# Optimization experiments

Measured on AMD Instinct MI355X. Metric: run time of the kernel, lower is better.

## Reference

```python
import jax, jax.numpy as jnp
import numpy as np

B, T, H, W = 4, 8, 256, 256


def _shift(u, axis, d):
    """Value at index i comes from i+d along `axis`; zero (Dirichlet) boundary."""
    if d == 0:
        return u
    pad = [(0, 0)] * u.ndim
    sl = [slice(None)] * u.ndim
    if d > 0:
        sl[axis] = slice(d, None)
        pad[axis] = (0, d)
    else:
        sl[axis] = slice(None, d)
        pad[axis] = (-d, 0)
    return jnp.pad(u[tuple(sl)], pad)


def custom_sigmoid(x, mn, mx):
    # matches NLL.custom_sigmoid: (sigmoid(x) + min/(max-min)) * (max-min)
    return (jax.nn.sigmoid(x) + mn / (mx - mn)) * (mx - mn)


def setup_inputs() -> dict:
    key = jax.random.key(0)
    k1, k2 = jax.random.split(key)
    x = jax.random.normal(k1, (B, T, H, W), dtype=jnp.float32)
    conv_w = jax.random.normal(k2, (8 * T, T, 3, 3), dtype=jnp.float32) * 0.05
    return {"x": x, "conv_w": conv_w}


def reference(x, conv_w):
    Bn, Tn, Hn, Wn = x.shape
    dt = dx = dy = 1.0  # st_lag = [1,1,1]

    # Encoder: Conv2d(n_t -> 8*n_t, 3x3, padding=1, bias=False)
    theta = jax.lax.conv_general_dilated(
        x, conv_w, window_strides=(1, 1), padding="SAME",
        dimension_numbers=("NCHW", "OIHW", "NCHW"))

    # reshape_params: split 8*n_t channels into SPDE fields, bounded to valid ranges
    kappa = custom_sigmoid(theta[:, :Tn], 0.01, 1.0)          # damping
    m1 = theta[:, Tn:2 * Tn]                                   # advection x
    m2 = theta[:, 2 * Tn:3 * Tn]                               # advection y
    Hxx = custom_sigmoid(theta[:, 3 * Tn:4 * Tn], 0.01, 1.0)  # diffusion tensor
    Hxy = 0.1 * jnp.tanh(theta[:, 4 * Tn:5 * Tn])
    Hyx = 0.1 * jnp.tanh(theta[:, 5 * Tn:6 * Tn])
    Hyy = custom_sigmoid(theta[:, 6 * Tn:7 * Tn], 0.01, 1.0)
    tau = custom_sigmoid(theta[:, 7 * Tn:8 * Tn], 0.1, 10.0)   # noise scale

    # finite-difference stencils (zero Dirichlet boundary), vectorized over (B,T)
    def Dx(u):
        return (_shift(u, -1, 1) - _shift(u, -1, -1)) / (2 * dx)

    def Dy(u):
        return (_shift(u, -2, 1) - _shift(u, -2, -1)) / (2 * dy)

    def Dxx(u):
        return (_shift(u, -1, 1) + _shift(u, -1, -1) - 2 * u) / (dx * dx)

    def Dyy(u):
        return (_shift(u, -2, 1) + _shift(u, -2, -1) - 2 * u) / (dy * dy)

    def A(u):
        # advection-diffusion operator: kappa^2 u + m.grad u - div(H grad u)
        return ((kappa * kappa) * u + m1 * Dx(u) + m2 * Dy(u)
                - (Hxx * Dxx(u) + Hyy * Dyy(u) + (Hxy + Hyx) * Dx(Dy(u))))

    # pow=1 -> alpha=2 -> B = A^2 ; M_k = I + dt * B_k
    Mx = x + dt * A(A(x))                      # [B,T,H,W], M_k x_k for all k

    # Q = L^T D L with L block-bidiagonal (L[k,k]=M_k, L[k,k-1]=-I),
    # D_k = diag(dt / tau_k^2)  (inv_tau = sqrt(dt)/tau in create_Q)
    x_prev = jnp.concatenate([jnp.zeros_like(x[:, :1]), x[:, :-1]], axis=1)
    r = Mx - x_prev                            # r_k = M_k x_k - x_{k-1}
    D = dt / (tau * tau)

    xQx = jnp.sum(D * r * r)                   # quadratic form x^T Q x
    logdetD = jnp.sum(jnp.log(D))              # diagonal log-det contribution
    return 0.5 * (xQx - logdetD)
```

## Files before the change

kernel.cpp:

```cpp
#include <hip/hip_runtime.h>

#define F_ELEMS 2097152
#define IMG 65536

typedef _Float16 half8  __attribute__((ext_vector_type(8)));
typedef _Float16 half2v __attribute__((ext_vector_type(2)));
typedef _Float16 half4v __attribute__((ext_vector_type(4)));
typedef float    floatx4 __attribute__((ext_vector_type(4)));

__device__ __forceinline__ float sigm(float x){ return 1.0f/(1.0f + __expf(-x)); }
__device__ __forceinline__ float tanh_fast(float x){
    float t = __expf(2.0f*x);
    return 1.0f - 2.0f/(t + 1.0f);
}

__global__ void zero_out(float* out){ out[0] = 0.0f; }

__global__ __launch_bounds__(256) void conv_mfma(
    const float* __restrict__ x, const float* __restrict__ w,
    _Float16* __restrict__ fld, float* __restrict__ out)
{
    __shared__ _Float16 xt[4*258*8];
    __shared__ _Float16 Wl[12*64*8];
    __shared__ float red[256];

    const int tid = threadIdx.x;
    const int i0  = blockIdx.x << 1;
    const int b   = blockIdx.y;

    for (int e = tid; e < 258*4*4; e += 256){
        int cc = e % 258;
        int rr = (e/258) & 3;
        int cp = e / (258*4);
        int gi = i0 - 1 + rr, gj = cc - 1;
        float v0 = 0.0f, v1 = 0.0f;
        if (gi >= 0 && gi < 256 && gj >= 0 && gj < 256){
            int base = ((b*8 + 2*cp) << 16) + (gi << 8) + gj;
            v0 = x[base];
            v1 = x[base + IMG];
        }
        half2v h; h[0] = (_Float16)v0; h[1] = (_Float16)v1;
        *(half2v*)&xt[(rr*258 + cc)*8 + 2*cp] = h;
    }
    for (int e = tid; e < 12*64*8; e += 256){
        int c  = e & 7;
        int oc = (e >> 3) & 63;
        int t  = e >> 9;
        float v = (t < 9) ? w[(oc*8 + c)*9 + t] : 0.0f;
        Wl[e] = (_Float16)v;
    }
    __syncthreads();

    const int lane = tid & 63;
    const int quad = lane >> 4;
    const int l16  = lane & 15;
    const int wv   = tid >> 6;

    half8 afr[4][3];
    int boff[3];
    #pragma unroll
    for (int s = 0; s < 3; ++s){
        int t  = s*4 + quad;
        afr[0][s] = *(const half8*)&Wl[(t*64 +  0 + l16)*8];
        afr[1][s] = *(const half8*)&Wl[(t*64 + 16 + l16)*8];
        afr[2][s] = *(const half8*)&Wl[(t*64 + 32 + l16)*8];
        afr[3][s] = *(const half8*)&Wl[(t*64 + 48 + l16)*8];
        int tc = (t < 9) ? t : 8;
        int dh = tc / 3, dw = tc - dh*3;
        boff[s] = (dh*258 + dw)*8;
    }

    float ldacc = 0.0f;

    #pragma unroll 2
    for (int it = 0; it < 8; ++it){
        const int g   = it*4 + wv;
        const int r   = g >> 4;
        const int jb  = ((g & 15) << 4) + l16;
        const int xoff = (r*258 + jb)*8;

        floatx4 acc0 = {0,0,0,0}, acc1 = {0,0,0,0}, acc2 = {0,0,0,0}, acc3 = {0,0,0,0};
        #pragma unroll
        for (int s = 0; s < 3; ++s){
            half8 bf = *(const half8*)&xt[xoff + boff[s]];
            acc0 = __builtin_amdgcn_mfma_f32_16x16x32_f16(afr[0][s], bf, acc0, 0, 0, 0);
            acc1 = __builtin_amdgcn_mfma_f32_16x16x32_f16(afr[1][s], bf, acc1, 0, 0, 0);
            acc2 = __builtin_amdgcn_mfma_f32_16x16x32_f16(afr[2][s], bf, acc2, 0, 0, 0);
            acc3 = __builtin_amdgcn_mfma_f32_16x16x32_f16(afr[3][s], bf, acc3, 0, 0, 0);
        }

        const int pix0 = (b << 19) + ((i0 + r) << 8) + jb;
#define STO(f, tt, v) fld[(f)*F_ELEMS + ((tt) << 16) + pix0] = (_Float16)(v)
        #pragma unroll
        for (int rg = 0; rg < 4; ++rg){
            int oc = quad*4 + rg, tt = oc & 7;
            float v = acc0[rg];
            if (oc < 8){ float s = 0.99f*sigm(v) + 0.01f; STO(0, tt, s*s); }
            else       { STO(1, tt, v); }
        }
        #pragma unroll
        for (int rg = 0; rg < 4; ++rg){
            int oc = 16 + quad*4 + rg, tt = oc & 7;
            float v = acc1[rg];
            if (oc < 24){ STO(2, tt, v); }
            else        { STO(3, tt, 0.99f*sigm(v) + 0.01f); }
        }
        #pragma unroll
        for (int rg = 0; rg < 4; ++rg){
            float th    = 0.1f*tanh_fast(acc2[rg]);
            float other = __shfl_xor(th, 32, 64);
            if (quad < 2){
                int tt = quad*4 + rg;
                STO(4, tt, th + other);
            }
        }
        #pragma unroll
        for (int rg = 0; rg < 4; ++rg){
            int oc = 48 + quad*4 + rg, tt = oc & 7;
            float v = acc3[rg];
            if (oc < 56){ STO(5, tt, 0.99f*sigm(v) + 0.01f); }
            else {
                float tau = 9.9f*sigm(v) + 0.1f;
                STO(6, tt, 1.0f/(tau*tau));
                ldacc += __logf(tau);
            }
        }
#undef STO
    }

    red[tid] = ldacc;
    __syncthreads();
    for (int s = 128; s > 0; s >>= 1){
        if (tid < s) red[tid] += red[tid + s];
        __syncthreads();
    }
    if (tid == 0) atomicAdd(out, red[0]);
}

__device__ __forceinline__ void ldf4(const _Float16* __restrict__ p, float o[4]){
    half4v h = *(const half4v*)p;
    o[0] = (float)h[0]; o[1] = (float)h[1]; o[2] = (float)h[2]; o[3] = (float)h[3];
}

__device__ __forceinline__ void row6(const float* __restrict__ u, int rb, int j0, float v[6]){
    const float4 c4 = *(const float4*)&u[rb + j0];
    v[1] = c4.x; v[2] = c4.y; v[3] = c4.z; v[4] = c4.w;
    v[0] = (j0 > 0)   ? u[rb + j0 - 1] : 0.0f;
    v[5] = (j0 < 252) ? u[rb + j0 + 4] : 0.0f;
}

__device__ __forceinline__ void stencil4(const float k2[4], const float m1[4],
    const float m2[4], const float hx[4], const float hs[4], const float hy[4],
    const float vc[6], const float vn[6], const float vs[6], float rp[4])
{
    #pragma unroll
    for (int p = 0; p < 4; ++p){
        float hxx = hx[p], hyy = hy[p];
        rp[p] = (k2[p] + 2.0f*(hxx + hyy))*vc[p+1]
              + (0.5f*m1[p] - hxx)*vc[p+2]
              - (0.5f*m1[p] + hxx)*vc[p]
              + (0.5f*m2[p] - hyy)*vn[p+1]
              - (0.5f*m2[p] + hyy)*vs[p+1]
              - 0.25f*hs[p]*(vn[p+2] - vs[p+2] - vn[p] + vs[p]);
    }
}

#define YSW 268
__global__ __launch_bounds__(256) void fused_A(
    const float* __restrict__ x, const _Float16* __restrict__ fld,
    float* __restrict__ out)
{
    __shared__ float ys[18*YSW];
    __shared__ float red[256];

    const int tid = threadIdx.x;
    const int cg  = tid & 63;
    const int rw  = tid >> 6;
    const int jc  = cg << 2;
    const int bt  = blockIdx.y;
    const int t   = bt & 7;
    const int i0  = blockIdx.x << 4;

    if (tid < 18){ ys[tid*YSW + 3] = 0.0f; ys[tid*YSW + 260] = 0.0f; }

    for (int p = 0; p < 5; ++p){
        int yr = p*4 + rw;
        if (yr < 18){
            int iy = i0 - 1 + yr;
            float y[4] = {0,0,0,0};
            if (iy >= 0 && iy < 256){
                int pix = (bt << 16) + (iy << 8) + jc;
                int rb  = pix - jc;
                float vc[6], vn[6], vs[6];
                row6(x, rb, jc, vc);
                if (iy < 255) row6(x, rb + 256, jc, vn);
                else { vn[0]=vn[1]=vn[2]=vn[3]=vn[4]=vn[5]=0.0f; }
                if (iy > 0) row6(x, rb - 256, jc, vs);
                else { vs[0]=vs[1]=vs[2]=vs[3]=vs[4]=vs[5]=0.0f; }
                float k2[4], m1[4], m2[4], hx[4], hs[4], hy[4];
                ldf4(&fld[0*F_ELEMS + pix], k2);
                ldf4(&fld[1*F_ELEMS + pix], m1);
                ldf4(&fld[2*F_ELEMS + pix], m2);
                ldf4(&fld[3*F_ELEMS + pix], hx);
                ldf4(&fld[4*F_ELEMS + pix], hs);
                ldf4(&fld[5*F_ELEMS + pix], hy);
                stencil4(k2, m1, m2, hx, hs, hy, vc, vn, vs, y);
            }
            float4 y4 = make_float4(y[0], y[1], y[2], y[3]);
            *(float4*)&ys[yr*YSW + 4 + jc] = y4;
        }
    }
    __syncthreads();

    float local = 0.0f;
    #pragma unroll
    for (int p = 0; p < 4; ++p){
        int zr = p*4 + rw;
        int iz = i0 + zr;
        int pix = (bt << 16) + (iz << 8) + jc;
        int base = (zr + 1)*YSW + 4 + jc;

        float vc[6], vn[6], vs[6];
        {
            float4 c4 = *(const float4*)&ys[base];
            vc[1]=c4.x; vc[2]=c4.y; vc[3]=c4.z; vc[4]=c4.w;
            vc[0]=ys[base-1]; vc[5]=ys[base+4];
            float4 n4 = *(const float4*)&ys[base+YSW];
            vn[1]=n4.x; vn[2]=n4.y; vn[3]=n4.z; vn[4]=n4.w;
            vn[0]=ys[base+YSW-1]; vn[5]=ys[base+YSW+4];
            float4 s4 = *(const float4*)&ys[base-YSW];
            vs[1]=s4.x; vs[2]=s4.y; vs[3]=s4.z; vs[4]=s4.w;
            vs[0]=ys[base-YSW-1]; vs[5]=ys[base-YSW+4];
        }
        float k2[4], m1[4], m2[4], hx[4], hs[4], hy[4], dv[4], z[4];
        ldf4(&fld[0*F_ELEMS + pix], k2);
        ldf4(&fld[1*F_ELEMS + pix], m1);
        ldf4(&fld[2*F_ELEMS + pix], m2);
        ldf4(&fld[3*F_ELEMS + pix], hx);
        ldf4(&fld[4*F_ELEMS + pix], hs);
        ldf4(&fld[5*F_ELEMS + pix], hy);
        ldf4(&fld[6*F_ELEMS + pix], dv);
        stencil4(k2, m1, m2, hx, hs, hy, vc, vn, vs, z);

        float4 xc = *(const float4*)&x[pix];
        float4 xp = make_float4(0,0,0,0);
        if (t > 0) xp = *(const float4*)&x[pix - IMG];
        const float* xcp = (const float*)&xc;
        const float* xpp = (const float*)&xp;
        #pragma unroll
        for (int q = 0; q < 4; ++q){
            float r = xcp[q] + z[q] - xpp[q];
            local += dv[q]*r*r;
        }
    }

    red[tid] = local;
    __syncthreads();
    for (int s = 128; s > 0; s >>= 1){
        if (tid < s) red[tid] += red[tid + s];
        __syncthreads();
    }
    if (tid == 0) atomicAdd(out, 0.5f*red[0]);
}

extern "C" void kernel_launch(void* const* d_in, const int* in_sizes, int n_in,
                              void* d_out, int out_size, void* d_ws, size_t ws_size,
                              hipStream_t stream)
{
    const float* x = (const float*)d_in[0];
    const float* w = (const float*)d_in[1];
    float* out = (float*)d_out;
    _Float16* fld = (_Float16*)d_ws;

    zero_out<<<1, 1, 0, stream>>>(out);
    conv_mfma<<<dim3(128, 4), 256, 0, stream>>>(x, w, fld, out);
    fused_A<<<dim3(16, 32), 256, 0, stream>>>(x, fld, out);
}
```

Before: 107.8 us.

## Move log-det into fused kernel, drop zero kernel, use wave-shuffle reductions

Removes the separate zero_out launch by having the first conv block zero the output, and stores tau directly instead of 1/tau^2 so the conv kernel no longer computes logs or runs its shared-memory tree reduction and atomic. The fused stencil kernel now computes 1/tau^2 and accumulates a per-thread product of tau whose log is added to the loss, and replaces its shared-memory tree reduction with wave-level shuffles plus a four-entry shared sum. This trades one launch and two barrier-heavy reductions for extra divides in the second kernel. Zeroing the output inside a block of the conv kernel relies on that kernel finishing before the fused kernel's atomics, which stream ordering guarantees. Storing tau in fp16 and multiplying many taus before the log carries some precision and overflow risk.

```diff
diff --git a/kernel.cpp b/kernel.cpp
--- a/kernel.cpp
+++ b/kernel.cpp
@@ -14,19 +14,18 @@
     return 1.0f - 2.0f/(t + 1.0f);
 }
 
-__global__ void zero_out(float* out){ out[0] = 0.0f; }
-
 __global__ __launch_bounds__(256) void conv_mfma(
     const float* __restrict__ x, const float* __restrict__ w,
     _Float16* __restrict__ fld, float* __restrict__ out)
 {
     __shared__ _Float16 xt[4*258*8];
     __shared__ _Float16 Wl[12*64*8];
-    __shared__ float red[256];
 
     const int tid = threadIdx.x;
     const int i0  = blockIdx.x << 1;
     const int b   = blockIdx.y;
+
+    if (tid == 0 && blockIdx.x == 0 && blockIdx.y == 0) out[0] = 0.0f;
 
     for (int e = tid; e < 258*4*4; e += 256){
         int cc = e % 258;
@@ -70,8 +69,6 @@
         boff[s] = (dh*258 + dw)*8;
     }
 
-    float ldacc = 0.0f;
-
     #pragma unroll 2
     for (int it = 0; it < 8; ++it){
         const int g   = it*4 + wv;
@@ -121,20 +118,11 @@
             if (oc < 56){ STO(5, tt, 0.99f*sigm(v) + 0.01f); }
             else {
                 float tau = 9.9f*sigm(v) + 0.1f;
-                STO(6, tt, 1.0f/(tau*tau));
-                ldacc += __logf(tau);
+                STO(6, tt, tau);
             }
         }
 #undef STO
     }
-
-    red[tid] = ldacc;
-    __syncthreads();
-    for (int s = 128; s > 0; s >>= 1){
-        if (tid < s) red[tid] += red[tid + s];
-        __syncthreads();
-    }
-    if (tid == 0) atomicAdd(out, red[0]);
 }
 
 __device__ __forceinline__ void ldf4(const _Float16* __restrict__ p, float o[4]){
@@ -171,7 +159,7 @@
     float* __restrict__ out)
 {
     __shared__ float ys[18*YSW];
-    __shared__ float red[256];
+    __shared__ float redA[4], redB[4];
 
     const int tid = threadIdx.x;
     const int cg  = tid & 63;
@@ -213,6 +201,7 @@
     __syncthreads();
 
     float local = 0.0f;
+    float lprod = 1.0f;
     #pragma unroll
     for (int p = 0; p < 4; ++p){
         int zr = p*4 + rw;
@@ -232,14 +221,14 @@
             vs[1]=s4.x; vs[2]=s4.y; vs[3]=s4.z; vs[4]=s4.w;
             vs[0]=ys[base-YSW-1]; vs[5]=ys[base-YSW+4];
         }
-        float k2[4], m1[4], m2[4], hx[4], hs[4], hy[4], dv[4], z[4];
+        float k2[4], m1[4], m2[4], hx[4], hs[4], hy[4], tv[4], z[4];
         ldf4(&fld[0*F_ELEMS + pix], k2);
         ldf4(&fld[1*F_ELEMS + pix], m1);
         ldf4(&fld[2*F_ELEMS + pix], m2);
         ldf4(&fld[3*F_ELEMS + pix], hx);
         ldf4(&fld[4*F_ELEMS + pix], hs);
         ldf4(&fld[5*F_ELEMS + pix], hy);
-        ldf4(&fld[6*F_ELEMS + pix], dv);
+        ldf4(&fld[6*F_ELEMS + pix], tv);
         stencil4(k2, m1, m2, hx, hs, hy, vc, vn, vs, z);
 
         float4 xc = *(const float4*)&x[pix];
@@ -250,17 +239,27 @@
         #pragma unroll
         for (int q = 0; q < 4; ++q){
             float r = xcp[q] + z[q] - xpp[q];
-            local += dv[q]*r*r;
-        }
-    }
-
-    red[tid] = local;
+            float dq = 1.0f/(tv[q]*tv[q]);
+            local += dq*r*r;
+        }
+        lprod *= tv[0]*tv[1];
+        lprod *= tv[2]*tv[3];
+    }
+
+    float a = local;
+    float b = __logf(lprod);
+    #pragma unroll
+    for (int off = 32; off > 0; off >>= 1){
+        a += __shfl_down(a, off);
+        b += __shfl_down(b, off);
+    }
+    if (cg == 0){ redA[rw] = a; redB[rw] = b; }
     __syncthreads();
-    for (int s = 128; s > 0; s >>= 1){
-        if (tid < s) red[tid] += red[tid + s];
-        __syncthreads();
-    }
-    if (tid == 0) atomicAdd(out, 0.5f*red[0]);
+    if (tid == 0){
+        float ra = redA[0] + redA[1] + redA[2] + redA[3];
+        float rb = redB[0] + redB[1] + redB[2] + redB[3];
+        atomicAdd(out, 0.5f*ra + rb);
+    }
 }
 
 extern "C" void kernel_launch(void* const* d_in, const int* in_sizes, int n_in,
@@ -272,7 +271,6 @@
     float* out = (float*)d_out;
     _Float16* fld = (_Float16*)d_ws;
 
-    zero_out<<<1, 1, 0, stream>>>(out);
     conv_mfma<<<dim3(128, 4), 256, 0, stream>>>(x, w, fld, out);
     fused_A<<<dim3(16, 32), 256, 0, stream>>>(x, fld, out);
 }
```

Measured after the change: 100.3 us. 6.9% less time.
